# Optimization experiments

Measured on AMD Instinct MI355X. Metric: run time of the kernel, lower is better.

The kernel has to match this reference:

```python
import jax, jax.numpy as jnp
import numpy as np
import math

E = 1024
H = 16
D = E // H  # head_dim = 64


def setup_inputs() -> dict:
    key = jax.random.key(0)
    ks = jax.random.split(key, 12)
    B, N = 2, 2048
    x = jax.random.normal(ks[0], (B, N, E), dtype=jnp.float32)
    region_mask = jax.random.randint(ks[1], (B, N), 0, 2).astype(jnp.float32)
    attn_mask = jax.random.randint(ks[2], (B, N, N), 0, 2).astype(bool)
    std = 0.02
    Wq = jax.random.normal(ks[3], (E, E), dtype=jnp.float32) * std
    Wk = jax.random.normal(ks[4], (E, E), dtype=jnp.float32) * std
    Wv = jax.random.normal(ks[5], (E, E), dtype=jnp.float32) * std
    Wo = jax.random.normal(ks[6], (E, E), dtype=jnp.float32) * std
    bq = jnp.zeros((E,), jnp.float32)
    bk = jnp.zeros((E,), jnp.float32)
    bv = jnp.zeros((E,), jnp.float32)
    bo = jnp.zeros((E,), jnp.float32)
    region_bias = jax.random.normal(ks[7], (1, H, 1, 1), dtype=jnp.float32) * std
    return {"x": x, "region_mask": region_mask, "attn_mask": attn_mask,
            "Wq": Wq, "bq": bq, "Wk": Wk, "bk": bk, "Wv": Wv, "bv": bv,
            "Wo": Wo, "bo": bo, "region_bias": region_bias}


def reference(x, region_mask, attn_mask, Wq, bq, Wk, bk, Wv, bv, Wo, bo, region_bias):
    B, N, _ = x.shape
    # projections (torch Linear: y = x @ W.T + b), split heads -> (B, H, N, D)
    def split_heads(y):
        return y.reshape(B, N, H, D).transpose(0, 2, 1, 3)
    q = split_heads(x @ Wq.T + bq)
    k = split_heads(x @ Wk.T + bk)
    v = split_heads(x @ Wv.T + bv)
    # eager scores (B, H, N, N)
    scores = jnp.einsum('bhqd,bhkd->bhqk', q, k) / math.sqrt(D)
    # additive regional bias: (1,H,1,1) * (B,1,N,1) broadcasts over keys
    scores = scores + region_bias * region_mask[:, None, :, None]
    # masked_fill(attn_mask, -inf); mask is (B,N,N) -> (B,1,N,N)
    scores = jnp.where(attn_mask[:, None, :, :], -jnp.inf, scores)
    w = jax.nn.softmax(scores, axis=-1)  # dropout is identity in eval
    out = jnp.einsum('bhqk,bhkd->bhqd', w, v)
    out = out.transpose(0, 2, 1, 3).reshape(B, N, E)
    return out @ Wo.T + bo
```

## Files before the change

### kernel.cpp

```cpp
#include <hip/hip_runtime.h>
#include <hip/hip_bf16.h>
#include <stdint.h>

typedef __hip_bfloat16 bf16;
typedef unsigned long long u64;
typedef __attribute__((ext_vector_type(4))) float f32x4;
typedef __attribute__((ext_vector_type(8))) short short8;

#define MFMA16 __builtin_amdgcn_mfma_f32_16x16x32_bf16

constexpr int Bc = 2, Nc = 2048, Ec = 1024, Hc = 16, Dc = 64;
constexpr int Mc = Bc * Nc;
constexpr int Kc = Ec;

constexpr size_t OFF_XB   = 256;
constexpr size_t SZ_XE    = (size_t)Mc * Ec * 2;
constexpr size_t SZ_W     = (size_t)Ec * Ec * 2;
constexpr size_t OFF_WQB  = OFF_XB  + SZ_XE;
constexpr size_t OFF_WKB  = OFF_WQB + SZ_W;
constexpr size_t OFF_WVB  = OFF_WKB + SZ_W;
constexpr size_t OFF_WOB  = OFF_WVB + SZ_W;
constexpr size_t OFF_QB   = OFF_WOB + SZ_W;
constexpr size_t OFF_KB   = OFF_QB  + SZ_XE;
constexpr size_t OFF_VTB  = OFF_KB  + SZ_XE;
constexpr size_t OFF_OB   = OFF_VTB + SZ_XE;
constexpr size_t OFF_MP   = OFF_OB  + SZ_XE;

#define QSCALE 0.18033688f

__device__ __forceinline__ void gld16(const void* g, void* l) {
  __builtin_amdgcn_global_load_lds((const __attribute__((address_space(1))) void*)g,
                                   (__attribute__((address_space(3))) void*)l,
                                   16, 0, 0);
}

__device__ __forceinline__ float fexp2(float x) {
#if __has_builtin(__builtin_amdgcn_exp2f)
  return __builtin_amdgcn_exp2f(x);
#else
  float r; asm("v_exp_f32 %0, %1" : "=v"(r) : "v"(x)); return r;
#endif
}

__device__ __forceinline__ unsigned cvt2(float a, float b) {
  __hip_bfloat162 h = __float22bfloat162_rn(float2{a, b});
  return *reinterpret_cast<unsigned*>(&h);
}

__device__ __forceinline__ unsigned nib4(unsigned x) {
  const unsigned b = ((x & 0x7F7F7F7Fu) + 0x7F7F7F7Fu) | x;
  return ((b >> 7) & 1u) | ((b >> 14) & 2u) | ((b >> 21) & 4u) | ((b >> 28) & 8u);
}

__global__ __launch_bounds__(256)
void prep(const unsigned char* __restrict__ mbytes,
          const float* __restrict__ x,  const float* __restrict__ wq,
          const float* __restrict__ wk, const float* __restrict__ wv,
          const float* __restrict__ wo,
          u64* __restrict__ packed,
          uint2* __restrict__ xb,  uint2* __restrict__ wqb,
          uint2* __restrict__ wkb, uint2* __restrict__ wvb,
          uint2* __restrict__ wob)
{
  if (blockIdx.x < 512) {
    __shared__ int found;
    if (threadIdx.x == 0) found = 0;
    __syncthreads();
    int loc = 0;
    for (int i = threadIdx.x; i < 4096; i += 256)
      if ((i & 3) && mbytes[i] == 1) loc = 1;
    if (loc) atomicOr(&found, 1);
    __syncthreads();
    const bool bytem = (found != 0);

    const int widx = blockIdx.x * 256 + threadIdx.x;
    u64 bits = 0;
    if (bytem) {
      const uint4* src = (const uint4*)(mbytes + (size_t)widx * 64);
#pragma unroll
      for (int i = 0; i < 4; ++i) {
        const uint4 v = src[i];
        bits |= (u64)nib4(v.x) << (16 * i + 0);
        bits |= (u64)nib4(v.y) << (16 * i + 4);
        bits |= (u64)nib4(v.z) << (16 * i + 8);
        bits |= (u64)nib4(v.w) << (16 * i + 12);
      }
    } else {
      const uint4* src = (const uint4*)mbytes + (size_t)widx * 16;
#pragma unroll
      for (int i = 0; i < 16; ++i) {
        const uint4 v = src[i];
        const unsigned n = (v.x != 0 ? 1u : 0u) | (v.y != 0 ? 2u : 0u) |
                           (v.z != 0 ? 4u : 0u) | (v.w != 0 ? 8u : 0u);
        bits |= (u64)n << (4 * i);
      }
    }
    packed[widx] = bits;
    return;
  }
  const long XG = (long)Mc * Ec / 4;
  const long WG = (long)Ec * Ec / 4;
  const long total = XG + 4 * WG;
  const long nthr = (long)(gridDim.x - 512) * 256;
  for (long g = (long)(blockIdx.x - 512) * 256 + threadIdx.x; g < total; g += nthr) {
    const float* src; uint2* dst; long r;
    if (g < XG)              { src = x;  dst = xb;  r = g; }
    else if (g < XG + WG)    { src = wq; dst = wqb; r = g - XG; }
    else if (g < XG + 2*WG)  { src = wk; dst = wkb; r = g - XG - WG; }
    else if (g < XG + 3*WG)  { src = wv; dst = wvb; r = g - XG - 2*WG; }
    else                     { src = wo; dst = wob; r = g - XG - 3*WG; }
    float4 v = reinterpret_cast<const float4*>(src)[r];
    uint2 o;
    o.x = cvt2(v.x, v.y);
    o.y = cvt2(v.z, v.w);
    dst[r] = o;
  }
}

template<int BN>
__device__ __forceinline__ void gemm_core(const bf16* __restrict__ A,
                                          const bf16* __restrict__ Bw,
                                          int bm, int bn,
                                          bf16* As0, bf16* As1,
                                          bf16* Bs0, bf16* Bs1,
                                          f32x4 (&acc)[4][BN / 32])
{
  constexpr int NJ = BN / 32;
  const int t = threadIdx.x, lane = t & 63, w = t >> 6;
  const int wr = w >> 1, wc = w & 1;
  const int llo = lane & 15, lhi = lane >> 4;
  const int srow = t >> 3, schunk = t & 7;
  const int sswz = schunk ^ (srow & 7);
  const bf16* aSrc = A  + (size_t)(bm * 128 + srow) * Kc + sswz * 8;
  const bf16* bSrc = Bw + (size_t)(bn * BN  + srow) * Kc + sswz * 8;

  auto stage = [&](bf16* Asb, bf16* Bsb, int kt) {
    char* ldsA = (char*)Asb + w * 1024;
    char* ldsB = (char*)Bsb + w * 1024;
#pragma unroll
    for (int i = 0; i < 4; ++i)
      gld16(aSrc + (size_t)i * 32 * Kc + kt, ldsA + i * 4096);
#pragma unroll
    for (int i = 0; i < BN / 32; ++i)
      gld16(bSrc + (size_t)i * 32 * Kc + kt, ldsB + i * 4096);
  };

  stage(As0, Bs0, 0);
  __syncthreads();

  for (int kti = 0; kti < Kc / 64; ++kti) {
    const bool even = !(kti & 1);
    const char* Asc = (const char*)(even ? As0 : As1);
    const char* Bsc = (const char*)(even ? Bs0 : Bs1);
    if (kti + 1 < Kc / 64)
      stage(even ? As1 : As0, even ? Bs1 : Bs0, (kti + 1) * 64);
#pragma unroll
    for (int kk = 0; kk < 2; ++kk) {
      short8 af[4], bg[NJ];
      const int chunk = (kk * 4 + lhi) ^ (lane & 7);
#pragma unroll
      for (int i = 0; i < 4; ++i) {
        const int rowa = wr * 64 + i * 16 + llo;
        af[i] = *(const short8*)(Asc + rowa * 128 + chunk * 16);
      }
#pragma unroll
      for (int j = 0; j < NJ; ++j) {
        const int rowb = wc * (BN / 2) + j * 16 + llo;
        bg[j] = *(const short8*)(Bsc + rowb * 128 + chunk * 16);
      }
#pragma unroll
      for (int i = 0; i < 4; ++i)
#pragma unroll
        for (int j = 0; j < NJ; ++j)
          acc[i][j] = MFMA16(af[i], bg[j], acc[i][j], 0, 0, 0);
    }
    __syncthreads();
  }
}

__global__ __launch_bounds__(256)
void gemm_qkv(const bf16* __restrict__ xb,
              const bf16* __restrict__ wq, const bf16* __restrict__ wk,
              const bf16* __restrict__ wv,
              const float* __restrict__ bq, const float* __restrict__ bk,
              const float* __restrict__ bv,
              bf16* __restrict__ Q, bf16* __restrict__ Ko, bf16* __restrict__ VT)
{
  __shared__ bf16 As[2][128 * 64], Bs[2][64 * 64];
  const int sel = blockIdx.x >> 9, inner = blockIdx.x & 511;
  const int bm = inner >> 4, bn = inner & 15;
  const bf16*  W    = sel == 0 ? wq : (sel == 1 ? wk : wv);
  const float* bias = sel == 0 ? bq : (sel == 1 ? bk : bv);
  f32x4 acc[4][2] = {};
  gemm_core<64>(xb, W, bm, bn, As[0], As[1], Bs[0], Bs[1], acc);

  const int t = threadIdx.x, lane = t & 63, w = t >> 6;
  const int wr = w >> 1, wc = w & 1;
  const int llo = lane & 15, lhi = lane >> 4;
#pragma unroll
  for (int i = 0; i < 4; ++i)
#pragma unroll
    for (int j = 0; j < 2; ++j)
#pragma unroll
      for (int r = 0; r < 4; ++r) {
        const int m = bm * 128 + wr * 64 + i * 16 + lhi * 4 + r;
        const int e = bn * 64 + wc * 32 + j * 16 + llo;
        float v = acc[i][j][r] + bias[e];
        if (sel == 0) {
          Q[(size_t)m * Ec + e] = __float2bfloat16(v * QSCALE);
        } else if (sel == 1) {
          Ko[(size_t)m * Ec + e] = __float2bfloat16(v);
        } else {
          const int b = m >> 11, n = m & 2047, h = e >> 6, d = e & 63;
          VT[(((size_t)(b * Hc + h)) * Dc + d) * Nc + n] = __float2bfloat16(v);
        }
      }
}

__global__ __launch_bounds__(256)
void gemm_out(const bf16* __restrict__ ob, const bf16* __restrict__ wo,
              const float* __restrict__ bo, float* __restrict__ out)
{
  __shared__ bf16 As[2][128 * 64], Bs[2][64 * 64];
  const int bm = blockIdx.x >> 4, bn = blockIdx.x & 15;
  f32x4 acc[4][2] = {};
  gemm_core<64>(ob, wo, bm, bn, As[0], As[1], Bs[0], Bs[1], acc);

  const int t = threadIdx.x, lane = t & 63, w = t >> 6;
  const int wr = w >> 1, wc = w & 1;
  const int llo = lane & 15, lhi = lane >> 4;
#pragma unroll
  for (int i = 0; i < 4; ++i)
#pragma unroll
    for (int j = 0; j < 2; ++j)
#pragma unroll
      for (int r = 0; r < 4; ++r) {
        const int m = bm * 128 + wr * 64 + i * 16 + lhi * 4 + r;
        const int e = bn * 64 + wc * 32 + j * 16 + llo;
        out[(size_t)m * Ec + e] = acc[i][j][r] + bo[e];
      }
}

__global__ __launch_bounds__(512, 4)
void flash_attn(const bf16* __restrict__ Q, const bf16* __restrict__ Kb,
                const bf16* __restrict__ VT, const u64* __restrict__ mpack,
                bf16* __restrict__ O)
{
  __shared__ bf16 Ks[2][64 * 64];
  __shared__ bf16 Vs[2][64 * 64];
  __shared__ bf16 Ps[8][16 * 64];
  const int t = threadIdx.x, lane = t & 63, w = t >> 6;
  const int bh = blockIdx.x >> 4, qt = blockIdx.x & 15;
  const int b = bh >> 4, h = bh & 15;
  const int q0 = qt * 128 + w * 16;
  const int llo = lane & 15, lhi = lane >> 4;
  const int swz = (lane & 7) << 4;

  short8 aq0, aq1;
  {
    const bf16* qb = Q + ((size_t)(b * Nc + q0 + llo)) * Ec + h * Dc + lhi * 8;
    aq0 = *(const short8*)qb;
    aq1 = *(const short8*)(qb + 32);
  }

  const short8 kOnes = {16256,16256,16256,16256,16256,16256,16256,16256};
  const f32x4 fz = {};
  f32x4 oacc[4] = {};
  f32x4 lacc = {};

  const int srow = t >> 3, schunk = t & 7;
  const int sswz = schunk ^ (srow & 7);
  const bf16* kSrc = Kb + ((size_t)(b * Nc + srow)) * Ec + h * Dc + sswz * 8;
  const bf16* vSrc = VT + ((size_t)(bh * Dc + srow)) * Nc + sswz * 8;

  const u64* mrow = mpack + ((size_t)(b * Nc) + q0 + llo) * (Nc / 64);

  auto stage = [&](int buf, int kt) {
    gld16(kSrc + (size_t)kt * Ec, (char*)Ks[buf] + w * 1024);
    gld16(vSrc + kt,              (char*)Vs[buf] + w * 1024);
  };

  char* prow = (char*)Ps[w] + llo * 128;

  auto body = [&](const char* KsC, const char* VsC, u64 mw) {
    f32x4 s[4];
    __builtin_amdgcn_s_setprio(1);
#pragma unroll
    for (int f = 0; f < 4; ++f) {
      const int row = f * 16 + llo;
      short8 kb0 = *(const short8*)(KsC + row * 128 + (((0 + lhi) * 16) ^ swz));
      short8 kb1 = *(const short8*)(KsC + row * 128 + (((4 + lhi) * 16) ^ swz));
      s[f] = MFMA16(kb0, aq0, fz, 0, 0, 0);
      s[f] = MFMA16(kb1, aq1, s[f], 0, 0, 0);
    }
    __builtin_amdgcn_s_setprio(0);

    const unsigned mlo = (unsigned)(mw >> (lhi * 4));
    const unsigned mhi = (unsigned)(mw >> (lhi * 4 + 32));
#pragma unroll
    for (int f = 0; f < 4; ++f) {
      const unsigned mf = (f < 2 ? (mlo >> (f * 16)) : (mhi >> ((f - 2) * 16)));
#pragma unroll
      for (int r = 0; r < 4; ++r) {
        const float p = fexp2(s[f][r]);
        s[f][r] = ((mf >> r) & 1u) ? 0.f : p;
      }
    }

#pragma unroll
    for (int f = 0; f < 4; ++f) {
      uint2 pk;
      pk.x = cvt2(s[f][0], s[f][1]);
      pk.y = cvt2(s[f][2], s[f][3]);
      *(uint2*)(prow + ((f * 32 + lhi * 8) ^ swz)) = pk;
    }
    asm volatile("s_waitcnt lgkmcnt(0)" ::: "memory");

    short8 pa0 = *(const short8*)(prow + ((0 * 64 + lhi * 16) ^ swz));
    short8 pa1 = *(const short8*)(prow + ((1 * 64 + lhi * 16) ^ swz));

    __builtin_amdgcn_s_setprio(1);
#pragma unroll
    for (int df = 0; df < 4; ++df) {
      const int row = df * 16 + llo;
      short8 vb0 = *(const short8*)(VsC + row * 128 + (((0 + lhi) * 16) ^ swz));
      short8 vb1 = *(const short8*)(VsC + row * 128 + (((4 + lhi) * 16) ^ swz));
      oacc[df] = MFMA16(pa0, vb0, oacc[df], 0, 0, 0);
      oacc[df] = MFMA16(pa1, vb1, oacc[df], 0, 0, 0);
    }
    lacc = MFMA16(pa0, kOnes, lacc, 0, 0, 0);
    lacc = MFMA16(pa1, kOnes, lacc, 0, 0, 0);
    __builtin_amdgcn_s_setprio(0);
  };

  stage(0, 0);
  __syncthreads();
  u64 mw = mrow[0];

  for (int ti = 0; ti < Nc / 64; ti += 2) {
    if (ti + 1 < Nc / 64) stage(1, (ti + 1) * 64);
    const u64 mwB = (ti + 1 < Nc / 64) ? mrow[ti + 1] : 0;
    body((const char*)Ks[0], (const char*)Vs[0], mw);
    __syncthreads();
    if (ti + 2 < Nc / 64) stage(0, (ti + 2) * 64);
    const u64 mwA = (ti + 2 < Nc / 64) ? mrow[ti + 2] : 0;
    body((const char*)Ks[1], (const char*)Vs[1], mwB);
    __syncthreads();
    mw = mwA;
  }

  float inv[4];
#pragma unroll
  for (int r = 0; r < 4; ++r) inv[r] = 1.0f / lacc[r];
#pragma unroll
  for (int df = 0; df < 4; ++df)
#pragma unroll
    for (int r = 0; r < 4; ++r) {
      const int q = q0 + lhi * 4 + r;
      const int e = h * Dc + df * 16 + llo;
      O[((size_t)(b * Nc + q)) * Ec + e] = __float2bfloat16(oacc[df][r] * inv[r]);
    }
}

extern "C" void kernel_launch(void* const* d_in, const int* in_sizes, int n_in,
                              void* d_out, int out_size, void* d_ws, size_t ws_size,
                              hipStream_t stream)
{
  (void)in_sizes; (void)n_in; (void)out_size; (void)ws_size;
  const float* x  = (const float*)d_in[0];
  const void* mask = d_in[2];
  const float* Wq = (const float*)d_in[3];
  const float* bq = (const float*)d_in[4];
  const float* Wk = (const float*)d_in[5];
  const float* bk = (const float*)d_in[6];
  const float* Wv = (const float*)d_in[7];
  const float* bv = (const float*)d_in[8];
  const float* Wo = (const float*)d_in[9];
  const float* bo = (const float*)d_in[10];
  float* out = (float*)d_out;
  char* ws = (char*)d_ws;

  bf16* XB  = (bf16*)(ws + OFF_XB);
  bf16* WQB = (bf16*)(ws + OFF_WQB);
  bf16* WKB = (bf16*)(ws + OFF_WKB);
  bf16* WVB = (bf16*)(ws + OFF_WVB);
  bf16* WOB = (bf16*)(ws + OFF_WOB);
  bf16* QB  = (bf16*)(ws + OFF_QB);
  bf16* KB  = (bf16*)(ws + OFF_KB);
  bf16* VTB = (bf16*)(ws + OFF_VTB);
  bf16* OB  = (bf16*)(ws + OFF_OB);
  u64*  MP  = (u64*)(ws + OFF_MP);

  prep<<<512 + 1280, 256, 0, stream>>>((const unsigned char*)mask,
                                       x, Wq, Wk, Wv, Wo, MP,
                                       (uint2*)XB, (uint2*)WQB, (uint2*)WKB,
                                       (uint2*)WVB, (uint2*)WOB);
  gemm_qkv<<<1536, 256, 0, stream>>>(XB, WQB, WKB, WVB, bq, bk, bv, QB, KB, VTB);
  flash_attn<<<512, 512, 0, stream>>>(QB, KB, VTB, MP, OB);
  gemm_out<<<512, 256, 0, stream>>>(OB, WOB, bo, out);
}
```

Measured before the change: 139.6 us.

## Split attention over key range into two halves and combine partial sums

The flash attention kernel becomes a template that can split the key sequence into two halves, doubling the block count from 512 to 1024. Each block writes unnormalized fp32 output partials and row sums to workspace, and a new combine kernel adds the two halves, normalizes, and writes bf16 output. The aim is more parallelism and better CU fill on a grid that was roughly one wave. The cost is extra fp32 partial traffic plus one more launch. The min-blocks launch-bounds hint is also dropped, which may change register allocation. The split path is used only when the workspace is large enough.

```diff
diff --git a/kernel.cpp b/kernel.cpp
--- a/kernel.cpp
+++ b/kernel.cpp
@@ -25,6 +25,11 @@
 constexpr size_t OFF_VTB  = OFF_KB  + SZ_XE;
 constexpr size_t OFF_OB   = OFF_VTB + SZ_XE;
 constexpr size_t OFF_MP   = OFF_OB  + SZ_XE;
+constexpr size_t OFF_PART = OFF_MP + (size_t)(Bc * Nc) * (Nc / 64) * 8;
+constexpr size_t SZ_PART  = (size_t)2 * 32 * Nc * Dc * 4;
+constexpr size_t OFF_LS   = OFF_PART + SZ_PART;
+constexpr size_t SZ_LS    = (size_t)2 * 32 * Nc * 4;
+constexpr size_t WS_NEED  = OFF_LS + SZ_LS;
 
 #define QSCALE 0.18033688f
 
@@ -241,20 +246,27 @@
       }
 }
 
-__global__ __launch_bounds__(512, 4)
+template<int NSPLIT>
+__global__ __launch_bounds__(512)
 void flash_attn(const bf16* __restrict__ Q, const bf16* __restrict__ Kb,
                 const bf16* __restrict__ VT, const u64* __restrict__ mpack,
-                bf16* __restrict__ O)
+                bf16* __restrict__ O, float* __restrict__ part,
+                float* __restrict__ lsum)
 {
   __shared__ bf16 Ks[2][64 * 64];
   __shared__ bf16 Vs[2][64 * 64];
   __shared__ bf16 Ps[8][16 * 64];
+  constexpr int NT = (Nc / 64) / NSPLIT;
   const int t = threadIdx.x, lane = t & 63, w = t >> 6;
-  const int bh = blockIdx.x >> 4, qt = blockIdx.x & 15;
+  const int inner = blockIdx.x & 511;
+  const int half = (NSPLIT == 2) ? (blockIdx.x >> 9) : 0;
+  const int bh = inner >> 4, qt = inner & 15;
   const int b = bh >> 4, h = bh & 15;
   const int q0 = qt * 128 + w * 16;
   const int llo = lane & 15, lhi = lane >> 4;
   const int swz = (lane & 7) << 4;
+  const int kt0 = half * (Nc / NSPLIT);
+  const int kw0 = kt0 >> 6;
 
   short8 aq0, aq1;
   {
@@ -333,40 +345,75 @@
     __builtin_amdgcn_s_setprio(0);
   };
 
-  stage(0, 0);
+  stage(0, kt0);
   __syncthreads();
-  u64 mw = mrow[0];
-
-  for (int ti = 0; ti < Nc / 64; ti += 2) {
-    if (ti + 1 < Nc / 64) stage(1, (ti + 1) * 64);
-    const u64 mwB = (ti + 1 < Nc / 64) ? mrow[ti + 1] : 0;
+  u64 mw = mrow[kw0];
+
+  for (int ti = 0; ti < NT; ti += 2) {
+    if (ti + 1 < NT) stage(1, kt0 + (ti + 1) * 64);
+    const u64 mwB = (ti + 1 < NT) ? mrow[kw0 + ti + 1] : 0;
     body((const char*)Ks[0], (const char*)Vs[0], mw);
     __syncthreads();
-    if (ti + 2 < Nc / 64) stage(0, (ti + 2) * 64);
-    const u64 mwA = (ti + 2 < Nc / 64) ? mrow[ti + 2] : 0;
+    if (ti + 2 < NT) stage(0, kt0 + (ti + 2) * 64);
+    const u64 mwA = (ti + 2 < NT) ? mrow[kw0 + ti + 2] : 0;
     body((const char*)Ks[1], (const char*)Vs[1], mwB);
     __syncthreads();
     mw = mwA;
   }
 
-  float inv[4];
-#pragma unroll
-  for (int r = 0; r < 4; ++r) inv[r] = 1.0f / lacc[r];
-#pragma unroll
-  for (int df = 0; df < 4; ++df)
-#pragma unroll
-    for (int r = 0; r < 4; ++r) {
-      const int q = q0 + lhi * 4 + r;
-      const int e = h * Dc + df * 16 + llo;
-      O[((size_t)(b * Nc + q)) * Ec + e] = __float2bfloat16(oacc[df][r] * inv[r]);
-    }
+  if constexpr (NSPLIT == 1) {
+    float inv[4];
+#pragma unroll
+    for (int r = 0; r < 4; ++r) inv[r] = 1.0f / lacc[r];
+#pragma unroll
+    for (int df = 0; df < 4; ++df)
+#pragma unroll
+      for (int r = 0; r < 4; ++r) {
+        const int q = q0 + lhi * 4 + r;
+        const int e = h * Dc + df * 16 + llo;
+        O[((size_t)(b * Nc + q)) * Ec + e] = __float2bfloat16(oacc[df][r] * inv[r]);
+      }
+  } else {
+    const size_t rowbase = ((size_t)half * 32 + bh) * Nc;
+#pragma unroll
+    for (int df = 0; df < 4; ++df)
+#pragma unroll
+      for (int r = 0; r < 4; ++r) {
+        const int q = q0 + lhi * 4 + r;
+        part[(rowbase + q) * Dc + df * 16 + llo] = oacc[df][r];
+      }
+    if (llo == 0) {
+#pragma unroll
+      for (int r = 0; r < 4; ++r)
+        lsum[rowbase + q0 + lhi * 4 + r] = lacc[r];
+    }
+  }
+}
+
+__global__ __launch_bounds__(256)
+void combine(const float* __restrict__ part, const float* __restrict__ lsum,
+             bf16* __restrict__ O)
+{
+  const int gid = blockIdx.x * 256 + threadIdx.x;
+  const int row = gid >> 4;
+  const int dq = gid & 15;
+  constexpr int ROWS = 32 * Nc;
+  const float4 p0 = *(const float4*)(part + (size_t)row * Dc + dq * 4);
+  const float4 p1 = *(const float4*)(part + ((size_t)ROWS + row) * Dc + dq * 4);
+  const float inv = 1.0f / (lsum[row] + lsum[ROWS + row]);
+  const int bh = row >> 11, n = row & 2047;
+  const int b = bh >> 4, h = bh & 15;
+  uint2 o;
+  o.x = cvt2((p0.x + p1.x) * inv, (p0.y + p1.y) * inv);
+  o.y = cvt2((p0.z + p1.z) * inv, (p0.w + p1.w) * inv);
+  *(uint2*)(O + ((size_t)(b * Nc + n)) * Ec + h * Dc + dq * 4) = o;
 }
 
 extern "C" void kernel_launch(void* const* d_in, const int* in_sizes, int n_in,
                               void* d_out, int out_size, void* d_ws, size_t ws_size,
                               hipStream_t stream)
 {
-  (void)in_sizes; (void)n_in; (void)out_size; (void)ws_size;
+  (void)in_sizes; (void)n_in; (void)out_size;
   const float* x  = (const float*)d_in[0];
   const void* mask = d_in[2];
   const float* Wq = (const float*)d_in[3];
@@ -390,12 +437,19 @@
   bf16* VTB = (bf16*)(ws + OFF_VTB);
   bf16* OB  = (bf16*)(ws + OFF_OB);
   u64*  MP  = (u64*)(ws + OFF_MP);
+  float* PART = (float*)(ws + OFF_PART);
+  float* LS   = (float*)(ws + OFF_LS);
 
   prep<<<512 + 1280, 256, 0, stream>>>((const unsigned char*)mask,
                                        x, Wq, Wk, Wv, Wo, MP,
                                        (uint2*)XB, (uint2*)WQB, (uint2*)WKB,
                                        (uint2*)WVB, (uint2*)WOB);
   gemm_qkv<<<1536, 256, 0, stream>>>(XB, WQB, WKB, WVB, bq, bk, bv, QB, KB, VTB);
-  flash_attn<<<512, 512, 0, stream>>>(QB, KB, VTB, MP, OB);
+  if (ws_size >= WS_NEED) {
+    flash_attn<2><<<1024, 512, 0, stream>>>(QB, KB, VTB, MP, OB, PART, LS);
+    combine<<<4096, 256, 0, stream>>>(PART, LS, OB);
+  } else {
+    flash_attn<1><<<512, 512, 0, stream>>>(QB, KB, VTB, MP, OB, PART, LS);
+  }
   gemm_out<<<512, 256, 0, stream>>>(OB, WOB, bo, out);
 }
```

Result: slower. 145.4 us (+4.1%).

## Process two 16-row query tiles per wave in flash attention to reuse K/V fragments

Applied to the files above, without the earlier changes.

Each wave of the flash attention kernel now handles 32 query rows (two 16-row MFMA tiles) instead of 16, so every K and V fragment read from LDS feeds twice as many MFMAs. The block drops to 256 threads (4 waves) with the same 128 queries per block, and each thread now issues two K and two V 16-byte loads per stage. This targets LDS read bandwidth and instruction overhead per MFMA. In exchange it roughly doubles accumulator and score registers, lowers the occupancy hint to 3, and leaves fewer waves per block to hide the exp and masking work.

```diff
diff --git a/kernel.cpp b/kernel.cpp
--- a/kernel.cpp
+++ b/kernel.cpp
@@ -241,124 +241,158 @@
       }
 }
 
-__global__ __launch_bounds__(512, 4)
+__global__ __launch_bounds__(256, 3)
 void flash_attn(const bf16* __restrict__ Q, const bf16* __restrict__ Kb,
                 const bf16* __restrict__ VT, const u64* __restrict__ mpack,
                 bf16* __restrict__ O)
 {
   __shared__ bf16 Ks[2][64 * 64];
   __shared__ bf16 Vs[2][64 * 64];
-  __shared__ bf16 Ps[8][16 * 64];
+  __shared__ bf16 Ps[4][32 * 64];
   const int t = threadIdx.x, lane = t & 63, w = t >> 6;
   const int bh = blockIdx.x >> 4, qt = blockIdx.x & 15;
   const int b = bh >> 4, h = bh & 15;
-  const int q0 = qt * 128 + w * 16;
+  const int q0 = qt * 128 + w * 32;
   const int llo = lane & 15, lhi = lane >> 4;
   const int swz = (lane & 7) << 4;
 
-  short8 aq0, aq1;
+  short8 aq00, aq01, aq10, aq11;
   {
-    const bf16* qb = Q + ((size_t)(b * Nc + q0 + llo)) * Ec + h * Dc + lhi * 8;
-    aq0 = *(const short8*)qb;
-    aq1 = *(const short8*)(qb + 32);
+    const bf16* qb0 = Q + ((size_t)(b * Nc + q0 + llo)) * Ec + h * Dc + lhi * 8;
+    aq00 = *(const short8*)qb0;
+    aq01 = *(const short8*)(qb0 + 32);
+    const bf16* qb1 = qb0 + (size_t)16 * Ec;
+    aq10 = *(const short8*)qb1;
+    aq11 = *(const short8*)(qb1 + 32);
   }
 
   const short8 kOnes = {16256,16256,16256,16256,16256,16256,16256,16256};
   const f32x4 fz = {};
-  f32x4 oacc[4] = {};
-  f32x4 lacc = {};
+  f32x4 oacc0[4] = {}, oacc1[4] = {};
+  f32x4 lacc0 = {}, lacc1 = {};
 
   const int srow = t >> 3, schunk = t & 7;
   const int sswz = schunk ^ (srow & 7);
   const bf16* kSrc = Kb + ((size_t)(b * Nc + srow)) * Ec + h * Dc + sswz * 8;
   const bf16* vSrc = VT + ((size_t)(bh * Dc + srow)) * Nc + sswz * 8;
 
-  const u64* mrow = mpack + ((size_t)(b * Nc) + q0 + llo) * (Nc / 64);
+  const u64* mrow0 = mpack + ((size_t)(b * Nc) + q0 + llo) * (Nc / 64);
+  const u64* mrow1 = mrow0 + (size_t)16 * (Nc / 64);
 
   auto stage = [&](int buf, int kt) {
-    gld16(kSrc + (size_t)kt * Ec, (char*)Ks[buf] + w * 1024);
-    gld16(vSrc + kt,              (char*)Vs[buf] + w * 1024);
+    gld16(kSrc + (size_t)kt * Ec,        (char*)Ks[buf] + w * 1024);
+    gld16(kSrc + (size_t)(kt + 32) * Ec, (char*)Ks[buf] + 4096 + w * 1024);
+    gld16(vSrc + kt,                     (char*)Vs[buf] + w * 1024);
+    gld16(vSrc + (size_t)32 * Nc + kt,   (char*)Vs[buf] + 4096 + w * 1024);
   };
 
-  char* prow = (char*)Ps[w] + llo * 128;
-
-  auto body = [&](const char* KsC, const char* VsC, u64 mw) {
-    f32x4 s[4];
+  char* prow0 = (char*)Ps[w] + llo * 128;
+  char* prow1 = prow0 + 16 * 128;
+
+  auto body = [&](const char* KsC, const char* VsC, u64 mw0, u64 mw1) {
+    f32x4 s0[4], s1[4];
     __builtin_amdgcn_s_setprio(1);
 #pragma unroll
     for (int f = 0; f < 4; ++f) {
       const int row = f * 16 + llo;
-      short8 kb0 = *(const short8*)(KsC + row * 128 + (((0 + lhi) * 16) ^ swz));
+      short8 kb0 = *(const short8*)(KsC + row * 128 + ((lhi * 16) ^ swz));
       short8 kb1 = *(const short8*)(KsC + row * 128 + (((4 + lhi) * 16) ^ swz));
-      s[f] = MFMA16(kb0, aq0, fz, 0, 0, 0);
-      s[f] = MFMA16(kb1, aq1, s[f], 0, 0, 0);
+      s0[f] = MFMA16(kb0, aq00, fz, 0, 0, 0);
+      s0[f] = MFMA16(kb1, aq01, s0[f], 0, 0, 0);
+      s1[f] = MFMA16(kb0, aq10, fz, 0, 0, 0);
+      s1[f] = MFMA16(kb1, aq11, s1[f], 0, 0, 0);
     }
     __builtin_amdgcn_s_setprio(0);
 
-    const unsigned mlo = (unsigned)(mw >> (lhi * 4));
-    const unsigned mhi = (unsigned)(mw >> (lhi * 4 + 32));
+    {
+      const unsigned mlo = (unsigned)(mw0 >> (lhi * 4));
+      const unsigned mhi = (unsigned)(mw0 >> (lhi * 4 + 32));
+#pragma unroll
+      for (int f = 0; f < 4; ++f) {
+        const unsigned mf = (f < 2 ? (mlo >> (f * 16)) : (mhi >> ((f - 2) * 16)));
+#pragma unroll
+        for (int r = 0; r < 4; ++r) {
+          const float p = fexp2(s0[f][r]);
+          s0[f][r] = ((mf >> r) & 1u) ? 0.f : p;
+        }
+      }
+    }
+    {
+      const unsigned mlo = (unsigned)(mw1 >> (lhi * 4));
+      const unsigned mhi = (unsigned)(mw1 >> (lhi * 4 + 32));
+#pragma unroll
+      for (int f = 0; f < 4; ++f) {
+        const unsigned mf = (f < 2 ? (mlo >> (f * 16)) : (mhi >> ((f - 2) * 16)));
+#pragma unroll
+        for (int r = 0; r < 4; ++r) {
+          const float p = fexp2(s1[f][r]);
+          s1[f][r] = ((mf >> r) & 1u) ? 0.f : p;
+        }
+      }
+    }
+
 #pragma unroll
     for (int f = 0; f < 4; ++f) {
-      const unsigned mf = (f < 2 ? (mlo >> (f * 16)) : (mhi >> ((f - 2) * 16)));
-#pragma unroll
-      for (int r = 0; r < 4; ++r) {
-        const float p = fexp2(s[f][r]);
-        s[f][r] = ((mf >> r) & 1u) ? 0.f : p;
-      }
-    }
-
-#pragma unroll
-    for (int f = 0; f < 4; ++f) {
-      uint2 pk;
-      pk.x = cvt2(s[f][0], s[f][1]);
-      pk.y = cvt2(s[f][2], s[f][3]);
-      *(uint2*)(prow + ((f * 32 + lhi * 8) ^ swz)) = pk;
+      uint2 pk0, pk1;
+      pk0.x = cvt2(s0[f][0], s0[f][1]); pk0.y = cvt2(s0[f][2], s0[f][3]);
+      pk1.x = cvt2(s1[f][0], s1[f][1]); pk1.y = cvt2(s1[f][2], s1[f][3]);
+      *(uint2*)(prow0 + ((f * 32 + lhi * 8) ^ swz)) = pk0;
+      *(uint2*)(prow1 + ((f * 32 + lhi * 8) ^ swz)) = pk1;
     }
     asm volatile("s_waitcnt lgkmcnt(0)" ::: "memory");
 
-    short8 pa0 = *(const short8*)(prow + ((0 * 64 + lhi * 16) ^ swz));
-    short8 pa1 = *(const short8*)(prow + ((1 * 64 + lhi * 16) ^ swz));
+    short8 pa00 = *(const short8*)(prow0 + ((lhi * 16) ^ swz));
+    short8 pa01 = *(const short8*)(prow0 + ((64 + lhi * 16) ^ swz));
+    short8 pa10 = *(const short8*)(prow1 + ((lhi * 16) ^ swz));
+    short8 pa11 = *(const short8*)(prow1 + ((64 + lhi * 16) ^ swz));
 
     __builtin_amdgcn_s_setprio(1);
 #pragma unroll
     for (int df = 0; df < 4; ++df) {
       const int row = df * 16 + llo;
-      short8 vb0 = *(const short8*)(VsC + row * 128 + (((0 + lhi) * 16) ^ swz));
+      short8 vb0 = *(const short8*)(VsC + row * 128 + ((lhi * 16) ^ swz));
       short8 vb1 = *(const short8*)(VsC + row * 128 + (((4 + lhi) * 16) ^ swz));
-      oacc[df] = MFMA16(pa0, vb0, oacc[df], 0, 0, 0);
-      oacc[df] = MFMA16(pa1, vb1, oacc[df], 0, 0, 0);
-    }
-    lacc = MFMA16(pa0, kOnes, lacc, 0, 0, 0);
-    lacc = MFMA16(pa1, kOnes, lacc, 0, 0, 0);
+      oacc0[df] = MFMA16(pa00, vb0, oacc0[df], 0, 0, 0);
+      oacc0[df] = MFMA16(pa01, vb1, oacc0[df], 0, 0, 0);
+      oacc1[df] = MFMA16(pa10, vb0, oacc1[df], 0, 0, 0);
+      oacc1[df] = MFMA16(pa11, vb1, oacc1[df], 0, 0, 0);
+    }
+    lacc0 = MFMA16(pa00, kOnes, lacc0, 0, 0, 0);
+    lacc0 = MFMA16(pa01, kOnes, lacc0, 0, 0, 0);
+    lacc1 = MFMA16(pa10, kOnes, lacc1, 0, 0, 0);
+    lacc1 = MFMA16(pa11, kOnes, lacc1, 0, 0, 0);
     __builtin_amdgcn_s_setprio(0);
   };
 
   stage(0, 0);
   __syncthreads();
-  u64 mw = mrow[0];
+  u64 mwA0 = mrow0[0], mwA1 = mrow1[0];
 
   for (int ti = 0; ti < Nc / 64; ti += 2) {
     if (ti + 1 < Nc / 64) stage(1, (ti + 1) * 64);
-    const u64 mwB = (ti + 1 < Nc / 64) ? mrow[ti + 1] : 0;
-    body((const char*)Ks[0], (const char*)Vs[0], mw);
+    const u64 mwB0 = (ti + 1 < Nc / 64) ? mrow0[ti + 1] : 0;
+    const u64 mwB1 = (ti + 1 < Nc / 64) ? mrow1[ti + 1] : 0;
+    body((const char*)Ks[0], (const char*)Vs[0], mwA0, mwA1);
     __syncthreads();
     if (ti + 2 < Nc / 64) stage(0, (ti + 2) * 64);
-    const u64 mwA = (ti + 2 < Nc / 64) ? mrow[ti + 2] : 0;
-    body((const char*)Ks[1], (const char*)Vs[1], mwB);
+    const u64 mwN0 = (ti + 2 < Nc / 64) ? mrow0[ti + 2] : 0;
+    const u64 mwN1 = (ti + 2 < Nc / 64) ? mrow1[ti + 2] : 0;
+    body((const char*)Ks[1], (const char*)Vs[1], mwB0, mwB1);
     __syncthreads();
-    mw = mwA;
+    mwA0 = mwN0; mwA1 = mwN1;
   }
 
-  float inv[4];
-#pragma unroll
-  for (int r = 0; r < 4; ++r) inv[r] = 1.0f / lacc[r];
+  float inv0[4], inv1[4];
+#pragma unroll
+  for (int r = 0; r < 4; ++r) { inv0[r] = 1.0f / lacc0[r]; inv1[r] = 1.0f / lacc1[r]; }
 #pragma unroll
   for (int df = 0; df < 4; ++df)
 #pragma unroll
     for (int r = 0; r < 4; ++r) {
-      const int q = q0 + lhi * 4 + r;
       const int e = h * Dc + df * 16 + llo;
-      O[((size_t)(b * Nc + q)) * Ec + e] = __float2bfloat16(oacc[df][r] * inv[r]);
+      const int qa = q0 + lhi * 4 + r;
+      O[((size_t)(b * Nc + qa)) * Ec + e] = __float2bfloat16(oacc0[df][r] * inv0[r]);
+      O[((size_t)(b * Nc + qa + 16)) * Ec + e] = __float2bfloat16(oacc1[df][r] * inv1[r]);
     }
 }
 
@@ -396,6 +430,6 @@
                                        (uint2*)XB, (uint2*)WQB, (uint2*)WKB,
                                        (uint2*)WVB, (uint2*)WOB);
   gemm_qkv<<<1536, 256, 0, stream>>>(XB, WQB, WKB, WVB, bq, bk, bv, QB, KB, VTB);
-  flash_attn<<<512, 512, 0, stream>>>(QB, KB, VTB, MP, OB);
+  flash_attn<<<512, 256, 0, stream>>>(QB, KB, VTB, MP, OB);
   gemm_out<<<512, 256, 0, stream>>>(OB, WOB, bo, out);
 }
```

Result: slower. 143.5 us (+2.7%).

## Fuse Q/K/V projections into one kernel sharing the staged X tile

Applied to the files above, without the earlier changes.

Replaces the three separate per-weight GEMM blocks (1536 blocks) with 512 blocks that each stage one 128-row X tile and compute against Wq, Wk and Wv tiles together. This reuses each A tile across three outputs, cutting global/LDS loads of X by a factor of three. In exchange each block holds three sets of accumulators, which raises register pressure, and needs larger LDS (B tiles for three weights). It also launches fewer blocks, which lowers parallelism on a 256-CU device.

```diff
diff --git a/kernel.cpp b/kernel.cpp
--- a/kernel.cpp
+++ b/kernel.cpp
@@ -117,6 +117,99 @@
   }
 }
 
+__global__ __launch_bounds__(256)
+void gemm_qkv(const bf16* __restrict__ xb,
+              const bf16* __restrict__ wq, const bf16* __restrict__ wk,
+              const bf16* __restrict__ wv,
+              const float* __restrict__ bq, const float* __restrict__ bk,
+              const float* __restrict__ bv,
+              bf16* __restrict__ Q, bf16* __restrict__ Ko, bf16* __restrict__ VT)
+{
+  __shared__ bf16 As[2][128 * 64];
+  __shared__ bf16 Bs[2][3][64 * 64];
+  const int bm = blockIdx.x >> 4, bn = blockIdx.x & 15;
+  const int t = threadIdx.x, lane = t & 63, w = t >> 6;
+  const int wr = w >> 1, wc = w & 1;
+  const int llo = lane & 15, lhi = lane >> 4;
+  const int srow = t >> 3, schunk = t & 7;
+  const int sswz = schunk ^ (srow & 7);
+  const bf16* aSrc  = xb + (size_t)(bm * 128 + srow) * Kc + sswz * 8;
+  const bf16* bSrc0 = wq + (size_t)(bn * 64 + srow) * Kc + sswz * 8;
+  const bf16* bSrc1 = wk + (size_t)(bn * 64 + srow) * Kc + sswz * 8;
+  const bf16* bSrc2 = wv + (size_t)(bn * 64 + srow) * Kc + sswz * 8;
+
+  f32x4 acc[3][4][2] = {};
+
+  auto stage = [&](int buf, int kt) {
+    char* ldsA = (char*)As[buf] + w * 1024;
+#pragma unroll
+    for (int i = 0; i < 4; ++i)
+      gld16(aSrc + (size_t)i * 32 * Kc + kt, ldsA + i * 4096);
+#pragma unroll
+    for (int s = 0; s < 3; ++s) {
+      const bf16* bs = s == 0 ? bSrc0 : (s == 1 ? bSrc1 : bSrc2);
+      char* ldsB = (char*)Bs[buf][s] + w * 1024;
+      gld16(bs + kt, ldsB);
+      gld16(bs + (size_t)32 * Kc + kt, ldsB + 4096);
+    }
+  };
+
+  stage(0, 0);
+  __syncthreads();
+
+  for (int kti = 0; kti < Kc / 64; ++kti) {
+    const int cur = kti & 1;
+    if (kti + 1 < Kc / 64) stage(cur ^ 1, (kti + 1) * 64);
+    const char* Asc = (const char*)As[cur];
+#pragma unroll
+    for (int kk = 0; kk < 2; ++kk) {
+      const int chunk = (kk * 4 + lhi) ^ (lane & 7);
+      short8 af[4];
+#pragma unroll
+      for (int i = 0; i < 4; ++i) {
+        const int rowa = wr * 64 + i * 16 + llo;
+        af[i] = *(const short8*)(Asc + rowa * 128 + chunk * 16);
+      }
+#pragma unroll
+      for (int s = 0; s < 3; ++s) {
+        const char* Bsc = (const char*)Bs[cur][s];
+        const int rowb0 = wc * 32 + llo;
+        short8 bg0 = *(const short8*)(Bsc + rowb0 * 128 + chunk * 16);
+        short8 bg1 = *(const short8*)(Bsc + (rowb0 + 16) * 128 + chunk * 16);
+#pragma unroll
+        for (int i = 0; i < 4; ++i) {
+          acc[s][i][0] = MFMA16(af[i], bg0, acc[s][i][0], 0, 0, 0);
+          acc[s][i][1] = MFMA16(af[i], bg1, acc[s][i][1], 0, 0, 0);
+        }
+      }
+    }
+    __syncthreads();
+  }
+
+#pragma unroll
+  for (int s = 0; s < 3; ++s) {
+    const float* bias = s == 0 ? bq : (s == 1 ? bk : bv);
+#pragma unroll
+    for (int i = 0; i < 4; ++i)
+#pragma unroll
+      for (int j = 0; j < 2; ++j)
+#pragma unroll
+        for (int r = 0; r < 4; ++r) {
+          const int m = bm * 128 + wr * 64 + i * 16 + lhi * 4 + r;
+          const int e = bn * 64 + wc * 32 + j * 16 + llo;
+          float v = acc[s][i][j][r] + bias[e];
+          if (s == 0) {
+            Q[(size_t)m * Ec + e] = __float2bfloat16(v * QSCALE);
+          } else if (s == 1) {
+            Ko[(size_t)m * Ec + e] = __float2bfloat16(v);
+          } else {
+            const int b = m >> 11, n = m & 2047, h = e >> 6, d = e & 63;
+            VT[(((size_t)(b * Hc + h)) * Dc + d) * Nc + n] = __float2bfloat16(v);
+          }
+        }
+  }
+}
+
 template<int BN>
 __device__ __forceinline__ void gemm_core(const bf16* __restrict__ A,
                                           const bf16* __restrict__ Bw,
@@ -176,45 +269,6 @@
     }
     __syncthreads();
   }
-}
-
-__global__ __launch_bounds__(256)
-void gemm_qkv(const bf16* __restrict__ xb,
-              const bf16* __restrict__ wq, const bf16* __restrict__ wk,
-              const bf16* __restrict__ wv,
-              const float* __restrict__ bq, const float* __restrict__ bk,
-              const float* __restrict__ bv,
-              bf16* __restrict__ Q, bf16* __restrict__ Ko, bf16* __restrict__ VT)
-{
-  __shared__ bf16 As[2][128 * 64], Bs[2][64 * 64];
-  const int sel = blockIdx.x >> 9, inner = blockIdx.x & 511;
-  const int bm = inner >> 4, bn = inner & 15;
-  const bf16*  W    = sel == 0 ? wq : (sel == 1 ? wk : wv);
-  const float* bias = sel == 0 ? bq : (sel == 1 ? bk : bv);
-  f32x4 acc[4][2] = {};
-  gemm_core<64>(xb, W, bm, bn, As[0], As[1], Bs[0], Bs[1], acc);
-
-  const int t = threadIdx.x, lane = t & 63, w = t >> 6;
-  const int wr = w >> 1, wc = w & 1;
-  const int llo = lane & 15, lhi = lane >> 4;
-#pragma unroll
-  for (int i = 0; i < 4; ++i)
-#pragma unroll
-    for (int j = 0; j < 2; ++j)
-#pragma unroll
-      for (int r = 0; r < 4; ++r) {
-        const int m = bm * 128 + wr * 64 + i * 16 + lhi * 4 + r;
-        const int e = bn * 64 + wc * 32 + j * 16 + llo;
-        float v = acc[i][j][r] + bias[e];
-        if (sel == 0) {
-          Q[(size_t)m * Ec + e] = __float2bfloat16(v * QSCALE);
-        } else if (sel == 1) {
-          Ko[(size_t)m * Ec + e] = __float2bfloat16(v);
-        } else {
-          const int b = m >> 11, n = m & 2047, h = e >> 6, d = e & 63;
-          VT[(((size_t)(b * Hc + h)) * Dc + d) * Nc + n] = __float2bfloat16(v);
-        }
-      }
 }
 
 __global__ __launch_bounds__(256)
@@ -395,7 +449,7 @@
                                        x, Wq, Wk, Wv, Wo, MP,
                                        (uint2*)XB, (uint2*)WQB, (uint2*)WKB,
                                        (uint2*)WVB, (uint2*)WOB);
-  gemm_qkv<<<1536, 256, 0, stream>>>(XB, WQB, WKB, WVB, bq, bk, bv, QB, KB, VTB);
+  gemm_qkv<<<512, 256, 0, stream>>>(XB, WQB, WKB, WVB, bq, bk, bv, QB, KB, VTB);
   flash_attn<<<512, 512, 0, stream>>>(QB, KB, VTB, MP, OB);
   gemm_out<<<512, 256, 0, stream>>>(OB, WOB, bo, out);
 }
```

After: 133.9 us. 1.04x faster.
